# Performance work log

Measured on AMD Instinct MI355X. Metric: run time of the kernel, lower is better.

Reference implementation:

```python
import jax, jax.numpy as jnp
import numpy as np

FRAMES, PATCHES, DIM, HEADS, DFF, K = 256, 64, 512, 8, 1024, 128


def _mhsa(x, Wqkv, Wo, h):
    # standard multi-head self-attention, no bias, no norm (as in the repo)
    b, t, d = x.shape
    dh = d // h
    qkv = x @ Wqkv                                   # [b, t, 3d]
    q, k, v = jnp.split(qkv, 3, axis=-1)
    rs = lambda z: z.reshape(b, t, h, dh).transpose(0, 2, 1, 3)  # [b,h,t,dh]
    q, k, v = rs(q), rs(k), rs(v)
    att = jax.nn.softmax(jnp.einsum('bhqd,bhkd->bhqk', q, k) * (dh ** -0.5), axis=-1)
    out = jnp.einsum('bhqk,bhkd->bhqd', att, v)
    return out.transpose(0, 2, 1, 3).reshape(b, t, d) @ Wo


def _linformer(x, Wqkv, Wo, E, h):
    # Linformer: project K and V along the token axis with E before attention
    b, t, d = x.shape
    dh = d // h
    qkv = x @ Wqkv
    q, k, v = jnp.split(qkv, 3, axis=-1)
    rs = lambda z: z.reshape(b, t, h, dh).transpose(0, 2, 1, 3)
    q, k, v = rs(q), rs(k), rs(v)
    k = jnp.einsum('bhjd,jk->bhkd', k, E)            # [b,h,K,dh]
    v = jnp.einsum('bhjd,jk->bhkd', v, E)
    att = jax.nn.softmax(jnp.einsum('bhqd,bhkd->bhqk', q, k) * (dh ** -0.5), axis=-1)
    out = jnp.einsum('bhqk,bhkd->bhqd', att, v)
    return out.transpose(0, 2, 1, 3).reshape(b, t, d) @ Wo


def setup_inputs() -> dict:
    key = jax.random.key(0)
    ks = jax.random.split(key, 10)
    s = 0.02
    n = 1 + FRAMES * PATCHES
    return {
        'x': jax.random.normal(ks[0], (1, n, DIM), jnp.float32),
        'Wqkv_t': jax.random.normal(ks[1], (DIM, 3 * DIM), jnp.float32) * s,
        'Wo_t': jax.random.normal(ks[2], (DIM, DIM), jnp.float32) * s,
        'Wqkv_s': jax.random.normal(ks[3], (DIM, 3 * DIM), jnp.float32) * s,
        'Wo_s': jax.random.normal(ks[4], (DIM, DIM), jnp.float32) * s,
        'E': jax.random.normal(ks[5], (PATCHES + 1, K), jnp.float32) * s,
        'W1': jax.random.normal(ks[6], (DIM, DFF), jnp.float32) * s,
        'b1': jnp.zeros((DFF,), jnp.float32),
        'W2': jax.random.normal(ks[7], (DFF, DIM), jnp.float32) * s,
        'b2': jnp.zeros((DIM,), jnp.float32),
    }


def reference(x, Wqkv_t, Wo_t, Wqkv_s, Wo_s, E, W1, b1, W2, b2):
    b, n, d = x.shape
    f, p = FRAMES, PATCHES
    # split cls token
    cls, xt = x[:, :1], x[:, 1:]                      # [b,1,d], [b,f*p,d]
    # rearrange 'b (f p) d -> (b p) f d'
    xt = xt.reshape(b, f, p, d).transpose(0, 2, 1, 3).reshape(b * p, f, d)
    cls_t = jnp.tile(cls, (b * p // b, 1, 1))          # expand cls to batch b*p
    xt = jnp.concatenate([cls_t, xt], axis=1)          # [b*p, f+1, d]
    y = _mhsa(xt, Wqkv_t, Wo_t, HEADS) + xt            # time attention + residual
    cls2, y = y[:, :1], y[:, 1:]                       # [b*p,1,d], [b*p,f,d]
    # rearrange '(b p) f d -> (b f) p d'
    y = y.reshape(b, p, f, d).transpose(0, 2, 1, 3).reshape(b * f, p, d)
    cls_s = jnp.tile(cls2, (b * f // (b * p), 1, 1))   # expand cls to batch b*f
    y = jnp.concatenate([cls_s, y], axis=1)            # [b*f, p+1, d]
    y = _linformer(y, Wqkv_s, Wo_s, E, HEADS) + y      # space attention + residual
    # rearrange '(b f) p d -> b (f p) d' (token count is p+1 here, per source)
    y = y.reshape(b, f * (p + 1), d)
    h = jax.nn.gelu(y @ W1 + b1, approximate=False)    # nn.GELU is exact erf
    y = (h @ W2 + b2) + y                              # MLP + residual (dropout=eval)
    return y
```

## Files before the change

kernel.cpp:

```cpp
#include <hip/hip_runtime.h>


typedef unsigned short u16;
typedef unsigned int   u32;
typedef __attribute__((ext_vector_type(8))) short s16x8;
typedef __attribute__((ext_vector_type(4))) float f32x4;

__device__ __forceinline__ float b2f(u16 u) {
    return __uint_as_float(((u32)u) << 16);
}
__device__ __forceinline__ u16 f2b(float f) {
    u32 v = __float_as_uint(f);
    return (u16)((v + 0x7FFFu + ((v >> 16) & 1u)) >> 16);
}

__device__ __forceinline__ void gload16(const u16* g, u16* l) {
    __builtin_amdgcn_global_load_lds(
        (const __attribute__((address_space(1))) u32*)(const void*)g,
        (__attribute__((address_space(3))) u32*)(void*)l, 16, 0, 0);
}

__global__ __launch_bounds__(128) void build_xt_k(const float* __restrict__ x,
                                                  u16* __restrict__ xt) {
    int row = blockIdx.x;
    int p = row / 257, t = row % 257;
    long src = (t == 0) ? 0L : (long)(1 + (t - 1) * 64 + p);
    float4 v = ((const float4*)(x + src * 512))[threadIdx.x];
    ushort4 o;
    o.x = f2b(v.x); o.y = f2b(v.y); o.z = f2b(v.z); o.w = f2b(v.w);
    ((ushort4*)(xt + (long)row * 512))[threadIdx.x] = o;
}

__global__ __launch_bounds__(128) void build_ys_k(const u16* __restrict__ yt,
                                                  u16* __restrict__ ys) {
    int row = blockIdx.x;
    int f = row / 65, s = row % 65;
    long src = (s == 0) ? (long)((f & 63) * 257) : (long)((s - 1) * 257 + 1 + f);
    const uint2* sp = (const uint2*)(yt + src * 512);
    ((uint2*)(ys + (long)row * 512))[threadIdx.x] = sp[threadIdx.x];
}

__global__ __launch_bounds__(256) void store_f32(const u16* __restrict__ src,
                                                 float* __restrict__ dst) {
    long i = ((long)blockIdx.x * 256 + threadIdx.x) * 8;
    uint4 v = *(const uint4*)(src + i);
    float4 a, b;
    a.x = b2f((u16)v.x); a.y = b2f((u16)(v.x >> 16));
    a.z = b2f((u16)v.y); a.w = b2f((u16)(v.y >> 16));
    b.x = b2f((u16)v.z); b.y = b2f((u16)(v.z >> 16));
    b.z = b2f((u16)v.w); b.w = b2f((u16)(v.w >> 16));
    *(float4*)(dst + i) = a;
    *(float4*)(dst + i + 4) = b;
}

__global__ __launch_bounds__(256) void prep_wt(const float* __restrict__ src,
                                               u16* __restrict__ dst,
                                               int K, int N) {
    __shared__ float T[64][65];
    int k0 = blockIdx.x * 64, n0 = blockIdx.y * 64;
    int t = threadIdx.x;
    int r = t >> 2, q = t & 3;
#pragma unroll
    for (int i = 0; i < 4; ++i) {
        float4 v = *(const float4*)(src + (long)(k0 + r) * N + n0 + q * 16 + i * 4);
        T[r][q * 16 + i * 4 + 0] = v.x;
        T[r][q * 16 + i * 4 + 1] = v.y;
        T[r][q * 16 + i * 4 + 2] = v.z;
        T[r][q * 16 + i * 4 + 3] = v.w;
    }
    __syncthreads();
    u32 buf[8];
#pragma unroll
    for (int i = 0; i < 8; ++i) {
        float lo = T[q * 16 + 2 * i][r];
        float hi = T[q * 16 + 2 * i + 1][r];
        buf[i] = (u32)f2b(lo) | ((u32)f2b(hi) << 16);
    }
    u32* dp = (u32*)(dst + (long)(n0 + r) * K + k0 + q * 16);
#pragma unroll
    for (int i = 0; i < 8; ++i) dp[i] = buf[i];
}

template <int EPI, int OD>
__global__ __launch_bounds__(256) void gemm_mt(const u16* __restrict__ A, int lda,
                                               const u16* __restrict__ WT, int ldwt,
                                               int koff, int coff,
                                               const float* __restrict__ bias, int coff_b,
                                               const u16* __restrict__ res,
                                               void* __restrict__ outv,
                                               int Kd, int ldo) {
    __shared__ __align__(16) u16 As3[2][64][32];
    __shared__ __align__(16) u16 Bs3[2][256][32];
    const int tid = threadIdx.x;
    const int lane = tid & 63, w = tid >> 6;
    const int l15 = lane & 15, kg = lane >> 4;
    const int bn0 = blockIdx.x * 256, bm0 = blockIdx.y * 64;

    f32x4 acc[4][4];
#pragma unroll
    for (int i = 0; i < 4; ++i)
#pragma unroll
        for (int j = 0; j < 4; ++j) acc[i][j] = (f32x4){0.f, 0.f, 0.f, 0.f};

    const int srow = w * 16 + (lane >> 2);
    const int sga  = (lane & 3) ^ ((srow >> 1) & 3);
    const u16* gA = A + (long)(bm0 + srow) * lda + sga * 8;
    const u16* gB[4];
#pragma unroll
    for (int i = 0; i < 4; ++i) {
        int scol = w * 64 + i * 16 + (lane >> 2);
        int sgb = (lane & 3) ^ ((scol >> 1) & 3);
        gB[i] = WT + (long)(coff + bn0 + scol) * ldwt + koff + sgb * 8;
    }

    gload16(gA, &As3[0][w * 16][0]);
#pragma unroll
    for (int i = 0; i < 4; ++i)
        gload16(gB[i], &Bs3[0][w * 64 + i * 16][0]);
    __syncthreads();

    int cur = 0;
    for (int kt = 0; kt < Kd; kt += 32) {
        if (kt + 32 < Kd) {
            gload16(gA + kt + 32, &As3[cur ^ 1][w * 16][0]);
#pragma unroll
            for (int i = 0; i < 4; ++i)
                gload16(gB[i] + kt + 32, &Bs3[cur ^ 1][w * 64 + i * 16][0]);
        }
        s16x8 af[4], bfr[4];
#pragma unroll
        for (int mf = 0; mf < 4; ++mf) {
            int row = mf * 16 + l15;
            int slot = kg ^ ((row >> 1) & 3);
            af[mf] = *(const s16x8*)&As3[cur][row][slot * 8];
        }
#pragma unroll
        for (int nf = 0; nf < 4; ++nf) {
            int col = w * 64 + nf * 16 + l15;
            int slot = kg ^ ((col >> 1) & 3);
            bfr[nf] = *(const s16x8*)&Bs3[cur][col][slot * 8];
        }
#pragma unroll
        for (int mf = 0; mf < 4; ++mf)
#pragma unroll
            for (int nf = 0; nf < 4; ++nf)
                acc[mf][nf] = __builtin_amdgcn_mfma_f32_16x16x32_bf16(
                    af[mf], bfr[nf], acc[mf][nf], 0, 0, 0);
        __syncthreads();
        cur ^= 1;
    }

#pragma unroll
    for (int mf = 0; mf < 4; ++mf) {
#pragma unroll
        for (int nf = 0; nf < 4; ++nf) {
            int col = bn0 + w * 64 + nf * 16 + l15;
#pragma unroll
            for (int r = 0; r < 4; ++r) {
                int row = bm0 + mf * 16 + kg * 4 + r;
                float v = acc[mf][nf][r];
                if (EPI == 2 || EPI == 3) v += bias[coff_b + col];
                if (EPI == 2) v = 0.5f * v * (1.f + erff(v * 0.70710678118f));
                if (EPI == 1 || EPI == 3) v += b2f(res[(long)row * ldo + col]);
                if (OD == 0) ((u16*)outv)[(long)row * ldo + col] = f2b(v);
                else         ((float*)outv)[(long)row * ldo + col] = v;
            }
        }
    }
}

template <int EPI, int OD>
__global__ __launch_bounds__(256) void gemm_k(const u16* __restrict__ A, int lda,
                                              const float* __restrict__ W, int ldw,
                                              int koff, int coff,
                                              const float* __restrict__ bias, int coff_b,
                                              const u16* __restrict__ res,
                                              void* __restrict__ outv,
                                              int M, int N, int Kd, int ldo) {
    __shared__ float As[16][64];
    __shared__ float Ws[16][128];
    int tid = threadIdx.x;
    int tx = tid & 15, ty = tid >> 4;
    int bn0 = blockIdx.x * 128, bm0 = blockIdx.y * 64;

    float acc[4][8];
#pragma unroll
    for (int i = 0; i < 4; ++i)
#pragma unroll
        for (int j = 0; j < 8; ++j) acc[i][j] = 0.f;

    int am = tid >> 2, ak = (tid & 3) * 4;
    int wk = tid >> 4, wn = (tid & 15) * 8;
    const u16* Aptr = A + (long)(bm0 + am) * lda + ak;

    for (int kt = 0; kt < Kd; kt += 16) {
        const u32* ap = (const u32*)(Aptr + kt);
        u32 a0 = ap[0], a1 = ap[1];
        const float* wp = W + (long)(koff + kt + wk) * ldw + coff + bn0 + wn;
        float4 w0 = ((const float4*)wp)[0];
        float4 w1 = ((const float4*)wp)[1];
        __syncthreads();
        As[ak + 0][am] = b2f((u16)a0);
        As[ak + 1][am] = b2f((u16)(a0 >> 16));
        As[ak + 2][am] = b2f((u16)a1);
        As[ak + 3][am] = b2f((u16)(a1 >> 16));
        Ws[wk][wn + 0] = w0.x; Ws[wk][wn + 1] = w0.y;
        Ws[wk][wn + 2] = w0.z; Ws[wk][wn + 3] = w0.w;
        Ws[wk][wn + 4] = w1.x; Ws[wk][wn + 5] = w1.y;
        Ws[wk][wn + 6] = w1.z; Ws[wk][wn + 7] = w1.w;
        __syncthreads();
#pragma unroll
        for (int kk = 0; kk < 16; ++kk) {
            float a[4], b[8];
#pragma unroll
            for (int i = 0; i < 4; ++i) a[i] = As[kk][ty + 16 * i];
#pragma unroll
            for (int j = 0; j < 8; ++j) b[j] = Ws[kk][tx + 16 * j];
#pragma unroll
            for (int i = 0; i < 4; ++i)
#pragma unroll
                for (int j = 0; j < 8; ++j) acc[i][j] += a[i] * b[j];
        }
    }

#pragma unroll
    for (int i = 0; i < 4; ++i) {
        int row = bm0 + ty + 16 * i;
#pragma unroll
        for (int j = 0; j < 8; ++j) {
            int col = bn0 + tx + 16 * j;
            float v = acc[i][j];
            if (EPI == 2 || EPI == 3) v += bias[coff_b + col];
            if (EPI == 2) v = 0.5f * v * (1.f + erff(v * 0.70710678118f));
            if (EPI == 1 || EPI == 3) v += b2f(res[(long)row * ldo + col]);
            if (OD == 0) ((u16*)outv)[(long)row * ldo + col] = f2b(v);
            else         ((float*)outv)[(long)row * ldo + col] = v;
        }
    }
}

__global__ __launch_bounds__(256) void attn_t3(u16* __restrict__ QO,
                                               const u16* __restrict__ Kg,
                                               const u16* __restrict__ Vg,
                                               int hbase, int qbase) {
    __shared__ __align__(16) u16 sm[17280];
    const int tid = threadIdx.x;
    const int lane = tid & 63, w = tid >> 6;
    const int l15 = lane & 15, kg = lane >> 4;
    const int seq = blockIdx.x >> 2, hq = blockIdx.x & 3, h = hbase + hq;
    const int qc = blockIdx.y;
    const long row0 = (long)seq * 257;
    const int qcol = qbase + hq * 64;
    const int rb = qc * 128 + w * 32;

    u16* Kb = sm;
    u16* Vb = sm + 4224;
    u16* Pw = sm + 8320 + w * 2240;

    const u32* Ku = (const u32*)Kg;
    const u32* Vu = (const u32*)Vg;

    s16x8 qf[2][2];
#pragma unroll
    for (int mf = 0; mf < 2; ++mf) {
        int row = rb + mf * 16 + l15;
#pragma unroll
        for (int ks = 0; ks < 2; ++ks) {
            if (row < 257)
                qf[mf][ks] = *(const s16x8*)(QO + (row0 + row) * 512 + qcol + ks * 32 + kg * 8);
            else
                qf[mf][ks] = (s16x8){0, 0, 0, 0, 0, 0, 0, 0};
        }
    }

    f32x4 acc_o[2][4];
    float m[2][4], l[2][4];
#pragma unroll
    for (int mf = 0; mf < 2; ++mf)
#pragma unroll
        for (int i = 0; i < 4; ++i) {
            acc_o[mf][i] = (f32x4){0.f, 0.f, 0.f, 0.f};
            m[mf][i] = -3.0e38f;
            l[mf][i] = 0.f;
        }

    for (int kc = 0; kc < 320; kc += 64) {
        __syncthreads();
        for (int idx = tid; idx < 2048; idx += 256) {
            int key = idx >> 5, cu = idx & 31, d0 = cu * 2;
            int kk = kc + key; if (kk > 256) kk = 256;
            u32 kv = Ku[(row0 + kk) * 256 + h * 32 + cu];
            *(u32*)&Kb[(((cu >> 2) * 66 + key) << 3) + (d0 & 7)] = kv;
        }
#pragma unroll
        for (int it = 0; it < 2; ++it) {
            int kg2 = (tid >> 6) + it * 4;
            int d = tid & 63;
            int sh = (d & 1) * 16;
            long vcol = hq * 32 + (d >> 1);
            u32 pk[4];
#pragma unroll
            for (int jp = 0; jp < 4; ++jp) {
                int k0 = kc + kg2 * 8 + 2 * jp;
                int k1 = k0 + 1;
                if (k0 > 256) k0 = 256;
                if (k1 > 256) k1 = 256;
                u32 a = Vu[(row0 + k0) * 128 + vcol];
                u32 b = Vu[(row0 + k1) * 128 + vcol];
                pk[jp] = ((a >> sh) & 0xFFFFu) | (((b >> sh) & 0xFFFFu) << 16);
            }
            uint4 vv; vv.x = pk[0]; vv.y = pk[1]; vv.z = pk[2]; vv.w = pk[3];
            *(uint4*)&Vb[(kg2 * 64 + d) << 3] = vv;
        }
        __syncthreads();

        s16x8 kbf[2][4];
#pragma unroll
        for (int ks = 0; ks < 2; ++ks)
#pragma unroll
            for (int nf = 0; nf < 4; ++nf)
                kbf[ks][nf] = *(const s16x8*)&Kb[(((ks * 4 + kg) * 66 + nf * 16 + l15) << 3)];

        const bool lastc = (kc == 256);
#pragma unroll
        for (int mf = 0; mf < 2; ++mf) {
            f32x4 accs[4];
#pragma unroll
            for (int nf = 0; nf < 4; ++nf) accs[nf] = (f32x4){0.f, 0.f, 0.f, 0.f};
#pragma unroll
            for (int ks = 0; ks < 2; ++ks)
#pragma unroll
                for (int nf = 0; nf < 4; ++nf)
                    accs[nf] = __builtin_amdgcn_mfma_f32_16x16x32_bf16(
                        qf[mf][ks], kbf[ks][nf], accs[nf], 0, 0, 0);
#pragma unroll
            for (int r = 0; r < 4; ++r) {
                float sv[4];
#pragma unroll
                for (int nf = 0; nf < 4; ++nf) sv[nf] = accs[nf][r] * 0.125f;
                if (lastc) {
#pragma unroll
                    for (int nf = 0; nf < 4; ++nf)
                        if (nf * 16 + l15 > 0) sv[nf] = -3.0e38f;
                }
                float mx = fmaxf(fmaxf(sv[0], sv[1]), fmaxf(sv[2], sv[3]));
                mx = fmaxf(mx, __shfl_xor(mx, 1));
                mx = fmaxf(mx, __shfl_xor(mx, 2));
                mx = fmaxf(mx, __shfl_xor(mx, 4));
                mx = fmaxf(mx, __shfl_xor(mx, 8));
                if (mx > m[mf][r] + 8.f) {
                    float sc = __expf(m[mf][r] - mx);
                    l[mf][r] *= sc;
#pragma unroll
                    for (int nf = 0; nf < 4; ++nf) acc_o[mf][nf][r] *= sc;
                    m[mf][r] = mx;
                }
                float pl = 0.f;
                u16 pb[4];
#pragma unroll
                for (int nf = 0; nf < 4; ++nf) {
                    float p = __expf(sv[nf] - m[mf][r]);
                    pl += p;
                    pb[nf] = f2b(p);
                }
                pl += __shfl_xor(pl, 1);
                pl += __shfl_xor(pl, 2);
                pl += __shfl_xor(pl, 4);
                pl += __shfl_xor(pl, 8);
                l[mf][r] += pl;
                const int rr = mf * 16 + kg * 4 + r;
#pragma unroll
                for (int nf = 0; nf < 4; ++nf)
                    Pw[(((nf * 2 + (l15 >> 3)) * 35 + rr) << 3) + (l15 & 7)] = pb[nf];
            }
        }
#pragma unroll
        for (int ks2 = 0; ks2 < 2; ++ks2) {
            s16x8 vbf[4];
#pragma unroll
            for (int nf = 0; nf < 4; ++nf)
                vbf[nf] = *(const s16x8*)&Vb[(((ks2 * 4 + kg) * 64 + nf * 16 + l15) << 3)];
#pragma unroll
            for (int mf = 0; mf < 2; ++mf) {
                s16x8 pa = *(const s16x8*)&Pw[(((ks2 * 4 + kg) * 35 + mf * 16 + l15) << 3)];
#pragma unroll
                for (int nf = 0; nf < 4; ++nf)
                    acc_o[mf][nf] = __builtin_amdgcn_mfma_f32_16x16x32_bf16(
                        pa, vbf[nf], acc_o[mf][nf], 0, 0, 0);
            }
        }
    }

#pragma unroll
    for (int mf = 0; mf < 2; ++mf) {
#pragma unroll
        for (int r = 0; r < 4; ++r) {
            int row = rb + mf * 16 + kg * 4 + r;
            if (row < 257) {
                float inv = 1.f / l[mf][r];
#pragma unroll
                for (int nf = 0; nf < 4; ++nf)
                    QO[(row0 + row) * 512 + qcol + nf * 16 + l15] =
                        f2b(acc_o[mf][nf][r] * inv);
            }
        }
    }
}

__global__ __launch_bounds__(320) void attn_t2(u16* __restrict__ QO,
                                               const u16* __restrict__ Kg,
                                               const u16* __restrict__ Vg,
                                               int hbase, int qbase_u32) {
    __shared__ u32 Ks[2080];
    __shared__ u32 Vs[2080];
    const int seq = blockIdx.x >> 2, hq = blockIdx.x & 3, h = hbase + hq;
    const int qc = blockIdx.y;
    const int tid = threadIdx.x;
    const int quad = tid >> 2, kq = tid & 3;
    const long row0 = (long)seq * 257;
    const int nq = (qc == 3) ? 65 : 64;
    const bool act = quad < nq;

    u32* QOu = (u32*)QO;
    const u32* Ku = (const u32*)Kg;
    const u32* Vu = (const u32*)Vg;

    const long qaddr = (row0 + qc * 64 + quad) * 256 + qbase_u32 + hq * 32 + kq * 8;

    float q[16], oacc[16];
#pragma unroll
    for (int i = 0; i < 16; ++i) { q[i] = 0.f; oacc[i] = 0.f; }
    if (act) {
        uint4 a = ((const uint4*)(QOu + qaddr))[0];
        uint4 b = ((const uint4*)(QOu + qaddr))[1];
        q[0]  = b2f((u16)a.x); q[1]  = b2f((u16)(a.x >> 16));
        q[2]  = b2f((u16)a.y); q[3]  = b2f((u16)(a.y >> 16));
        q[4]  = b2f((u16)a.z); q[5]  = b2f((u16)(a.z >> 16));
        q[6]  = b2f((u16)a.w); q[7]  = b2f((u16)(a.w >> 16));
        q[8]  = b2f((u16)b.x); q[9]  = b2f((u16)(b.x >> 16));
        q[10] = b2f((u16)b.y); q[11] = b2f((u16)(b.y >> 16));
        q[12] = b2f((u16)b.z); q[13] = b2f((u16)(b.z >> 16));
        q[14] = b2f((u16)b.w); q[15] = b2f((u16)(b.w >> 16));
    }
    float m = -3.0e38f, l = 0.f;

    for (int cc = 0; cc < 4; ++cc) {
        const int c0 = cc << 6;
        const int cn = (cc == 3) ? 65 : 64;
        __syncthreads();
        for (int idx = tid; idx < (cn << 5); idx += 320) {
            int r = idx >> 5, c = idx & 31;
            long grow = row0 + c0 + r;
            Ks[idx] = Ku[grow * 256 + h * 32 + c];
            Vs[idx] = Vu[grow * 128 + hq * 32 + c];
        }
        __syncthreads();
        if (act) {
            for (int j = 0; j < cn; ++j) {
                const uint4* kp = (const uint4*)(Ks + (j << 5) + (kq << 3));
                uint4 ka = kp[0], kb = kp[1];
                float s =
                    q[0]  * b2f((u16)ka.x) + q[1]  * b2f((u16)(ka.x >> 16)) +
                    q[2]  * b2f((u16)ka.y) + q[3]  * b2f((u16)(ka.y >> 16)) +
                    q[4]  * b2f((u16)ka.z) + q[5]  * b2f((u16)(ka.z >> 16)) +
                    q[6]  * b2f((u16)ka.w) + q[7]  * b2f((u16)(ka.w >> 16)) +
                    q[8]  * b2f((u16)kb.x) + q[9]  * b2f((u16)(kb.x >> 16)) +
                    q[10] * b2f((u16)kb.y) + q[11] * b2f((u16)(kb.y >> 16)) +
                    q[12] * b2f((u16)kb.z) + q[13] * b2f((u16)(kb.z >> 16)) +
                    q[14] * b2f((u16)kb.w) + q[15] * b2f((u16)(kb.w >> 16));
                s += __shfl_xor(s, 1);
                s += __shfl_xor(s, 2);
                s *= 0.125f;
                if (s > m + 8.f) {
                    float sc = __expf(m - s);
                    l *= sc;
#pragma unroll
                    for (int i = 0; i < 16; ++i) oacc[i] *= sc;
                    m = s;
                }
                float p = __expf(s - m);
                l += p;
                const uint4* vp = (const uint4*)(Vs + (j << 5) + (kq << 3));
                uint4 va = vp[0], vb = vp[1];
                oacc[0]  += p * b2f((u16)va.x); oacc[1]  += p * b2f((u16)(va.x >> 16));
                oacc[2]  += p * b2f((u16)va.y); oacc[3]  += p * b2f((u16)(va.y >> 16));
                oacc[4]  += p * b2f((u16)va.z); oacc[5]  += p * b2f((u16)(va.z >> 16));
                oacc[6]  += p * b2f((u16)va.w); oacc[7]  += p * b2f((u16)(va.w >> 16));
                oacc[8]  += p * b2f((u16)vb.x); oacc[9]  += p * b2f((u16)(vb.x >> 16));
                oacc[10] += p * b2f((u16)vb.y); oacc[11] += p * b2f((u16)(vb.y >> 16));
                oacc[12] += p * b2f((u16)vb.z); oacc[13] += p * b2f((u16)(vb.z >> 16));
                oacc[14] += p * b2f((u16)vb.w); oacc[15] += p * b2f((u16)(vb.w >> 16));
            }
        }
    }
    if (act) {
        float inv = 1.f / l;
        uint4 o0, o1;
        o0.x = (u32)f2b(oacc[0]  * inv) | ((u32)f2b(oacc[1]  * inv) << 16);
        o0.y = (u32)f2b(oacc[2]  * inv) | ((u32)f2b(oacc[3]  * inv) << 16);
        o0.z = (u32)f2b(oacc[4]  * inv) | ((u32)f2b(oacc[5]  * inv) << 16);
        o0.w = (u32)f2b(oacc[6]  * inv) | ((u32)f2b(oacc[7]  * inv) << 16);
        o1.x = (u32)f2b(oacc[8]  * inv) | ((u32)f2b(oacc[9]  * inv) << 16);
        o1.y = (u32)f2b(oacc[10] * inv) | ((u32)f2b(oacc[11] * inv) << 16);
        o1.z = (u32)f2b(oacc[12] * inv) | ((u32)f2b(oacc[13] * inv) << 16);
        o1.w = (u32)f2b(oacc[14] * inv) | ((u32)f2b(oacc[15] * inv) << 16);
        ((uint4*)(QOu + qaddr))[0] = o0;
        ((uint4*)(QOu + qaddr))[1] = o1;
    }
}

__global__ __launch_bounds__(320) void attn_s2(const u16* __restrict__ Qg,
                                               const u16* __restrict__ Kg,
                                               u16* __restrict__ Vg,
                                               const float* __restrict__ E,
                                               int hbase) {
    __shared__ u32 smu[14882];
    u32* Kpt = smu;
    u32* Es2 = smu + 4352;
    u32* Ks2 = smu + 8512;
    u32* Vs2 = smu + 10592;
    u32* Qs2 = smu + 12672;

    const int bid = blockIdx.x, f = bid >> 2, hq = bid & 3, h = hbase + hq;
    const int tid = threadIdx.x;
    const long rbase = (long)f * 65;
    const u32* Kgu = (const u32*)Kg;
    u32* Vgu = (u32*)Vg;
    const u32* Qgu = (const u32*)Qg;

    for (int idx = tid; idx < 4160; idx += 320) {
        float e0 = E[2 * idx], e1 = E[2 * idx + 1];
        Es2[idx] = (u32)f2b(e0) | ((u32)f2b(e1) << 16);
    }
    for (int idx = tid; idx < 2080; idx += 320) {
        int r = idx >> 5, c = idx & 31;
        long src = (rbase + r) * 256 + h * 32 + c;
        Ks2[r * 32 + c] = Kgu[src];
        Vs2[r * 32 + c] = Vgu[src];
        Qs2[r * 34 + c] = Qgu[(rbase + r) * 128 + hq * 32 + c];
    }
    __syncthreads();

    if (tid < 256) {
        const int d = tid >> 2, kq4 = tid & 3;
        float kp[32];
#pragma unroll
        for (int i = 0; i < 32; ++i) kp[i] = 0.f;
        const u16* Ku = (const u16*)Ks2;
        for (int j = 0; j < 65; ++j) {
            float kv = b2f(Ku[j * 64 + d]);
            const uint4* ep = (const uint4*)(Es2 + j * 64 + kq4 * 16);
#pragma unroll
            for (int i4 = 0; i4 < 4; ++i4) {
                uint4 e4 = ep[i4];
                kp[i4 * 8 + 0] += kv * b2f((u16)e4.x);
                kp[i4 * 8 + 1] += kv * b2f((u16)(e4.x >> 16));
                kp[i4 * 8 + 2] += kv * b2f((u16)e4.y);
                kp[i4 * 8 + 3] += kv * b2f((u16)(e4.y >> 16));
                kp[i4 * 8 + 4] += kv * b2f((u16)e4.z);
                kp[i4 * 8 + 5] += kv * b2f((u16)(e4.z >> 16));
                kp[i4 * 8 + 6] += kv * b2f((u16)e4.w);
                kp[i4 * 8 + 7] += kv * b2f((u16)(e4.w >> 16));
            }
        }
        u32* ko = Kpt + d * 68 + kq4 * 16;
#pragma unroll
        for (int i2 = 0; i2 < 16; ++i2)
            ko[i2] = (u32)f2b(kp[2 * i2]) | ((u32)f2b(kp[2 * i2 + 1]) << 16);
    }
    __syncthreads();

    const int q = tid >> 2, kq = tid & 3;
    if (q < 65) {
        float s[32];
#pragma unroll
        for (int i = 0; i < 32; ++i) s[i] = 0.f;
        const u32* qrow = Qs2 + q * 34;
        for (int d2 = 0; d2 < 32; ++d2) {
            u32 qw = qrow[d2];
            float q0 = b2f((u16)qw), q1 = b2f((u16)(qw >> 16));
            const uint4* r0 = (const uint4*)(Kpt + (2 * d2) * 68 + kq * 16);
            const uint4* r1 = (const uint4*)(Kpt + (2 * d2 + 1) * 68 + kq * 16);
#pragma unroll
            for (int i4 = 0; i4 < 4; ++i4) {
                uint4 a = r0[i4], b = r1[i4];
                s[i4 * 8 + 0] += q0 * b2f((u16)a.x) + q1 * b2f((u16)b.x);
                s[i4 * 8 + 1] += q0 * b2f((u16)(a.x >> 16)) + q1 * b2f((u16)(b.x >> 16));
                s[i4 * 8 + 2] += q0 * b2f((u16)a.y) + q1 * b2f((u16)b.y);
                s[i4 * 8 + 3] += q0 * b2f((u16)(a.y >> 16)) + q1 * b2f((u16)(b.y >> 16));
                s[i4 * 8 + 4] += q0 * b2f((u16)a.z) + q1 * b2f((u16)b.z);
                s[i4 * 8 + 5] += q0 * b2f((u16)(a.z >> 16)) + q1 * b2f((u16)(b.z >> 16));
                s[i4 * 8 + 6] += q0 * b2f((u16)a.w) + q1 * b2f((u16)b.w);
                s[i4 * 8 + 7] += q0 * b2f((u16)(a.w >> 16)) + q1 * b2f((u16)(b.w >> 16));
            }
        }
        float m = -3.0e38f;
#pragma unroll
        for (int i = 0; i < 32; ++i) { s[i] *= 0.125f; m = fmaxf(m, s[i]); }
        m = fmaxf(m, __shfl_xor(m, 1));
        m = fmaxf(m, __shfl_xor(m, 2));
        float l = 0.f;
#pragma unroll
        for (int i = 0; i < 32; ++i) { s[i] = __expf(s[i] - m); l += s[i]; }
        l += __shfl_xor(l, 1);
        l += __shfl_xor(l, 2);

        float o[16];
#pragma unroll
        for (int i = 0; i < 16; ++i) o[i] = 0.f;
        for (int j = 0; j < 65; ++j) {
            const uint4* ep = (const uint4*)(Es2 + j * 64 + kq * 16);
            float pe = 0.f;
#pragma unroll
            for (int i4 = 0; i4 < 4; ++i4) {
                uint4 e4 = ep[i4];
                pe += s[i4 * 8 + 0] * b2f((u16)e4.x) + s[i4 * 8 + 1] * b2f((u16)(e4.x >> 16))
                    + s[i4 * 8 + 2] * b2f((u16)e4.y) + s[i4 * 8 + 3] * b2f((u16)(e4.y >> 16))
                    + s[i4 * 8 + 4] * b2f((u16)e4.z) + s[i4 * 8 + 5] * b2f((u16)(e4.z >> 16))
                    + s[i4 * 8 + 6] * b2f((u16)e4.w) + s[i4 * 8 + 7] * b2f((u16)(e4.w >> 16));
            }
            pe += __shfl_xor(pe, 1);
            pe += __shfl_xor(pe, 2);
            const uint4* vp = (const uint4*)(Vs2 + j * 32 + kq * 8);
#pragma unroll
            for (int i4 = 0; i4 < 2; ++i4) {
                uint4 v4 = vp[i4];
                o[i4 * 8 + 0] += pe * b2f((u16)v4.x);
                o[i4 * 8 + 1] += pe * b2f((u16)(v4.x >> 16));
                o[i4 * 8 + 2] += pe * b2f((u16)v4.y);
                o[i4 * 8 + 3] += pe * b2f((u16)(v4.y >> 16));
                o[i4 * 8 + 4] += pe * b2f((u16)v4.z);
                o[i4 * 8 + 5] += pe * b2f((u16)(v4.z >> 16));
                o[i4 * 8 + 6] += pe * b2f((u16)v4.w);
                o[i4 * 8 + 7] += pe * b2f((u16)(v4.w >> 16));
            }
        }
        float inv = 1.f / l;
        u32* op = Vgu + (rbase + q) * 256 + h * 32 + kq * 8;
#pragma unroll
        for (int i = 0; i < 8; ++i)
            op[i] = (u32)f2b(o[2 * i] * inv) | ((u32)f2b(o[2 * i + 1] * inv) << 16);
    }
}

__global__ __launch_bounds__(256) void attn_s3(const u16* __restrict__ Qg,
                                               const u16* __restrict__ Kg,
                                               u16* __restrict__ Vg,
                                               const float* __restrict__ E,
                                               int hbase) {
    __shared__ __align__(16) u16 sm[33024];
    u16* ET8 = sm;
    u16* KT8 = sm + 8192;
    u16* VT8 = sm + 12288;
    u16* Er  = sm + 16384;
    u16* Kr  = sm + 16512;
    u16* Vr  = sm + 16576;
    u16* Q8  = sm;
    u16* P16 = sm + 5120;
    float* Srow = (float*)(sm + 15360);
    u16* Kp8   = sm + 16640;
    u16* VpT16 = sm + 24832;

    const int bid = blockIdx.x, f = bid >> 2, hq = bid & 3, h = hbase + hq;
    const int tid = threadIdx.x;
    const int lane = tid & 63, w = tid >> 6;
    const int l15 = lane & 15, kg = lane >> 4;
    const long rbase = (long)f * 65;
    const u32* Kgu = (const u32*)Kg;
    u32* Vgu = (u32*)Vg;
    const u32* Qgu = (const u32*)Qg;

    for (int idx = tid; idx < 8320; idx += 256) {
        int j = idx >> 7, kL = idx & 127;
        u16 v = f2b(E[idx]);
        if (j < 64) ET8[(((j >> 3) * 128 + kL) << 3) + (j & 7)] = v;
        else        Er[kL] = v;
    }
    for (int idx = tid; idx < 2080; idx += 256) {
        int j = idx >> 5, cu = idx & 31;
        long src = (rbase + j) * 256 + h * 32 + cu;
        u32 kv = Kgu[src], vv = Vgu[src];
        int d0 = cu * 2;
        if (j < 64) {
            int base = (j >> 3), jj = j & 7;
            KT8[(((base) * 64 + d0) << 3) + jj]     = (u16)kv;
            KT8[(((base) * 64 + d0 + 1) << 3) + jj] = (u16)(kv >> 16);
            VT8[(((base) * 64 + d0) << 3) + jj]     = (u16)vv;
            VT8[(((base) * 64 + d0 + 1) << 3) + jj] = (u16)(vv >> 16);
        } else {
            Kr[d0] = (u16)kv; Kr[d0 + 1] = (u16)(kv >> 16);
            Vr[d0] = (u16)vv; Vr[d0 + 1] = (u16)(vv >> 16);
        }
    }
    __syncthreads();

    {
        f32x4 acc[2][4];
#pragma unroll
        for (int i = 0; i < 2; ++i)
#pragma unroll
            for (int j2 = 0; j2 < 4; ++j2) acc[i][j2] = (f32x4){0.f, 0.f, 0.f, 0.f};
#pragma unroll
        for (int ks = 0; ks < 2; ++ks) {
            int c = ks * 4 + kg;
            s16x8 a0 = *(const s16x8*)&ET8[((c * 128 + (2 * w) * 16 + l15) << 3)];
            s16x8 a1 = *(const s16x8*)&ET8[((c * 128 + (2 * w + 1) * 16 + l15) << 3)];
            s16x8 b0 = *(const s16x8*)&KT8[((c * 64 + 0 * 16 + l15) << 3)];
            s16x8 b1 = *(const s16x8*)&KT8[((c * 64 + 1 * 16 + l15) << 3)];
            s16x8 b2v = *(const s16x8*)&KT8[((c * 64 + 2 * 16 + l15) << 3)];
            s16x8 b3 = *(const s16x8*)&KT8[((c * 64 + 3 * 16 + l15) << 3)];
            acc[0][0] = __builtin_amdgcn_mfma_f32_16x16x32_bf16(a0, b0, acc[0][0], 0, 0, 0);
            acc[0][1] = __builtin_amdgcn_mfma_f32_16x16x32_bf16(a0, b1, acc[0][1], 0, 0, 0);
            acc[0][2] = __builtin_amdgcn_mfma_f32_16x16x32_bf16(a0, b2v, acc[0][2], 0, 0, 0);
            acc[0][3] = __builtin_amdgcn_mfma_f32_16x16x32_bf16(a0, b3, acc[0][3], 0, 0, 0);
            acc[1][0] = __builtin_amdgcn_mfma_f32_16x16x32_bf16(a1, b0, acc[1][0], 0, 0, 0);
            acc[1][1] = __builtin_amdgcn_mfma_f32_16x16x32_bf16(a1, b1, acc[1][1], 0, 0, 0);
            acc[1][2] = __builtin_amdgcn_mfma_f32_16x16x32_bf16(a1, b2v, acc[1][2], 0, 0, 0);
            acc[1][3] = __builtin_amdgcn_mfma_f32_16x16x32_bf16(a1, b3, acc[1][3], 0, 0, 0);
        }
#pragma unroll
        for (int mi = 0; mi < 2; ++mi)
#pragma unroll
            for (int nf = 0; nf < 4; ++nf) {
                int d = nf * 16 + l15;
                float kr = b2f(Kr[d]);
                int cidx = (nf * 2 + (l15 >> 3));
#pragma unroll
                for (int r = 0; r < 4; ++r) {
                    int kL = (2 * w + mi) * 16 + kg * 4 + r;
                    float v = acc[mi][nf][r] + b2f(Er[kL]) * kr;
                    Kp8[((cidx * 128 + kL) << 3) + (l15 & 7)] = f2b(v);
                }
            }
    }

    {
        f32x4 acc[8];
#pragma unroll
        for (int i = 0; i < 8; ++i) acc[i] = (f32x4){0.f, 0.f, 0.f, 0.f};
#pragma unroll
        for (int ks = 0; ks < 2; ++ks) {
            int c = ks * 4 + kg;
            s16x8 a = *(const s16x8*)&VT8[((c * 64 + w * 16 + l15) << 3)];
#pragma unroll
            for (int nf = 0; nf < 8; ++nf) {
                s16x8 b = *(const s16x8*)&ET8[((c * 128 + nf * 16 + l15) << 3)];
                acc[nf] = __builtin_amdgcn_mfma_f32_16x16x32_bf16(a, b, acc[nf], 0, 0, 0);
            }
        }
#pragma unroll
        for (int nf = 0; nf < 8; ++nf) {
            int kL = nf * 16 + l15;
            float er = b2f(Er[kL]);
            int cidx = (nf * 2 + (l15 >> 3));
#pragma unroll
            for (int r = 0; r < 4; ++r) {
                int d = w * 16 + kg * 4 + r;
                float v = acc[nf][r] + b2f(Vr[d]) * er;
                VpT16[((cidx * 64 + d) << 3) + (l15 & 7)] = f2b(v);
            }
        }
    }
    __syncthreads();

    for (int idx = tid; idx < 2560; idx += 256) {
        int rq = idx >> 5, cu = idx & 31;
        u32 val = (rq < 65) ? Qgu[(rbase + rq) * 128 + hq * 32 + cu] : 0u;
        *(u32*)&Q8[(((cu >> 2) * 80 + rq) << 3) + ((2 * cu) & 7)] = val;
    }
    __syncthreads();

    {
        f32x4 accs[8], acc4[2];
#pragma unroll
        for (int i = 0; i < 8; ++i) accs[i] = (f32x4){0.f, 0.f, 0.f, 0.f};
#pragma unroll
        for (int i = 0; i < 2; ++i) acc4[i] = (f32x4){0.f, 0.f, 0.f, 0.f};
#pragma unroll
        for (int ks = 0; ks < 2; ++ks) {
            int c = ks * 4 + kg;
            s16x8 a = *(const s16x8*)&Q8[((c * 80 + w * 16 + l15) << 3)];
            s16x8 a4 = *(const s16x8*)&Q8[((c * 80 + 64 + l15) << 3)];
#pragma unroll
            for (int nf = 0; nf < 8; ++nf) {
                s16x8 b = *(const s16x8*)&Kp8[((c * 128 + nf * 16 + l15) << 3)];
                accs[nf] = __builtin_amdgcn_mfma_f32_16x16x32_bf16(a, b, accs[nf], 0, 0, 0);
            }
#pragma unroll
            for (int i = 0; i < 2; ++i) {
                int nf4 = 2 * w + i;
                s16x8 b = *(const s16x8*)&Kp8[((c * 128 + nf4 * 16 + l15) << 3)];
                acc4[i] = __builtin_amdgcn_mfma_f32_16x16x32_bf16(a4, b, acc4[i], 0, 0, 0);
            }
        }
#pragma unroll
        for (int r = 0; r < 4; ++r) {
            float sv[8];
            float mx = -3.0e38f;
#pragma unroll
            for (int nf = 0; nf < 8; ++nf) {
                sv[nf] = accs[nf][r] * 0.125f;
                mx = fmaxf(mx, sv[nf]);
            }
            mx = fmaxf(mx, __shfl_xor(mx, 1));
            mx = fmaxf(mx, __shfl_xor(mx, 2));
            mx = fmaxf(mx, __shfl_xor(mx, 4));
            mx = fmaxf(mx, __shfl_xor(mx, 8));
            float l = 0.f;
#pragma unroll
            for (int nf = 0; nf < 8; ++nf) { sv[nf] = __expf(sv[nf] - mx); l += sv[nf]; }
            l += __shfl_xor(l, 1);
            l += __shfl_xor(l, 2);
            l += __shfl_xor(l, 4);
            l += __shfl_xor(l, 8);
            float inv = 1.f / l;
            int row = w * 16 + kg * 4 + r;
#pragma unroll
            for (int nf = 0; nf < 8; ++nf)
                P16[(((nf * 2 + (l15 >> 3)) * 80 + row) << 3) + (l15 & 7)] = f2b(sv[nf] * inv);
        }
        if (kg == 0) {
#pragma unroll
            for (int i = 0; i < 2; ++i)
                Srow[(2 * w + i) * 16 + l15] = acc4[i][0] * 0.125f;
        }
        for (int idx = tid; idx < 1920; idx += 256) {
            int row = 65 + (idx >> 7), col = idx & 127;
            P16[(((col >> 3) * 80 + row) << 3) + (col & 7)] = 0;
        }
    }
    __syncthreads();

    if (w == 0) {
        float v0 = Srow[lane], v1 = Srow[lane + 64];
        float mx = fmaxf(v0, v1);
#pragma unroll
        for (int s = 1; s < 64; s <<= 1) mx = fmaxf(mx, __shfl_xor(mx, s));
        float p0 = __expf(v0 - mx), p1 = __expf(v1 - mx);
        float l = p0 + p1;
#pragma unroll
        for (int s = 1; s < 64; s <<= 1) l += __shfl_xor(l, s);
        float inv = 1.f / l;
        int c0 = lane, c1 = lane + 64;
        P16[(((c0 >> 3) * 80 + 64) << 3) + (c0 & 7)] = f2b(p0 * inv);
        P16[(((c1 >> 3) * 80 + 64) << 3) + (c1 & 7)] = f2b(p1 * inv);
    }
    __syncthreads();

    {
        f32x4 acco[4], acco4;
#pragma unroll
        for (int i = 0; i < 4; ++i) acco[i] = (f32x4){0.f, 0.f, 0.f, 0.f};
        acco4 = (f32x4){0.f, 0.f, 0.f, 0.f};
#pragma unroll
        for (int ks = 0; ks < 4; ++ks) {
            int c = ks * 4 + kg;
            s16x8 a = *(const s16x8*)&P16[((c * 80 + w * 16 + l15) << 3)];
            s16x8 a4 = *(const s16x8*)&P16[((c * 80 + 64 + l15) << 3)];
#pragma unroll
            for (int nf = 0; nf < 4; ++nf) {
                s16x8 b = *(const s16x8*)&VpT16[((c * 64 + nf * 16 + l15) << 3)];
                acco[nf] = __builtin_amdgcn_mfma_f32_16x16x32_bf16(a, b, acco[nf], 0, 0, 0);
            }
            s16x8 b4 = *(const s16x8*)&VpT16[((c * 64 + w * 16 + l15) << 3)];
            acco4 = __builtin_amdgcn_mfma_f32_16x16x32_bf16(a4, b4, acco4, 0, 0, 0);
        }
        u16* Vg16 = (u16*)Vgu;
#pragma unroll
        for (int nf = 0; nf < 4; ++nf) {
            int d = nf * 16 + l15;
#pragma unroll
            for (int r = 0; r < 4; ++r) {
                int q = w * 16 + kg * 4 + r;
                Vg16[(rbase + q) * 512 + h * 64 + d] = f2b(acco[nf][r]);
            }
        }
        if (kg == 0) {
            int d = w * 16 + l15;
            Vg16[(rbase + 64) * 512 + h * 64 + d] = f2b(acco4[0]);
        }
    }
}

extern "C" void kernel_launch(void* const* d_in, const int* in_sizes, int n_in,
                              void* d_out, int out_size, void* d_ws, size_t ws_size,
                              hipStream_t stream) {
    int ix = 0, iE = 5, ib1 = 7, ib2 = 9;
    int q1 = -1, q2 = -1, o1 = -1, o2 = -1, w1 = -1, w2 = -1;
    for (int i = 0; i < n_in; ++i) {
        int s = in_sizes[i];
        if (s == 8389120) { if (ix != i && i == 0) ix = i; else if (in_sizes[ix] != 8389120) ix = i; }
        else if (s == 8320) iE = i;
        else if (s == 1024) ib1 = i;
        else if (s == 512) ib2 = i;
        else if (s == 786432) { if (q1 < 0) q1 = i; else q2 = i; }
        else if (s == 262144) { if (o1 < 0) o1 = i; else o2 = i; }
        else if (s == 524288) { if (w1 < 0) w1 = i; else w2 = i; }
    }
    if (q1 < 0) q1 = 1; if (o1 < 0) o1 = 2;
    if (q2 < 0) q2 = 3; if (o2 < 0) o2 = 4;
    if (w1 < 0) w1 = 6; if (ib1 < 0) ib1 = 7;
    if (w2 < 0) w2 = 8;

    const float* x      = (const float*)d_in[ix];
    const float* Wqkv_t = (const float*)d_in[q1];
    const float* Wo_t   = (const float*)d_in[o1];
    const float* Wqkv_s = (const float*)d_in[q2];
    const float* Wo_s   = (const float*)d_in[o2];
    const float* E      = (const float*)d_in[iE];
    const float* W1     = (const float*)d_in[w1];
    const float* b1     = (const float*)d_in[ib1];
    const float* W2     = (const float*)d_in[w2];
    const float* b2     = (const float*)d_in[ib2];

    float* outf = (float*)d_out;
    u16* D0 = (u16*)d_out;
    u16* B = (u16*)d_ws;
    u16* H = B + 8519680L;
    u16* D0up = D0 + 8519680L;

    const bool mfma = (ws_size >= 31850496UL);

    if (mfma) {
        u16* WT1 = H + 4259840L;
        u16* WT2 = WT1 + 786432L;
        u16* WT3 = WT2 + 262144L;
        u16* WT4 = WT3 + 786432L;
        u16* WT5 = WT4 + 262144L;
        u16* WT6 = WT5 + 524288L;

        prep_wt<<<dim3(8, 24), 256, 0, stream>>>(Wqkv_t, WT1, 512, 1536);
        prep_wt<<<dim3(8, 8),  256, 0, stream>>>(Wo_t,   WT2, 512, 512);
        prep_wt<<<dim3(8, 24), 256, 0, stream>>>(Wqkv_s, WT3, 512, 1536);
        prep_wt<<<dim3(8, 8),  256, 0, stream>>>(Wo_s,   WT4, 512, 512);
        prep_wt<<<dim3(8, 16), 256, 0, stream>>>(W1,     WT5, 512, 1024);
        prep_wt<<<dim3(16, 8), 256, 0, stream>>>(W2,     WT6, 1024, 512);

        build_xt_k<<<16448, 128, 0, stream>>>(x, B);
        gemm_mt<0, 0><<<dim3(2, 257), 256, 0, stream>>>(B, 512, WT1, 512, 0, 512,
                                                        nullptr, 0, nullptr, D0up, 512, 512);
        gemm_mt<0, 0><<<dim3(2, 257), 256, 0, stream>>>(B, 512, WT1, 512, 0, 0,
                                                        nullptr, 0, nullptr, D0, 512, 512);
        gemm_mt<0, 0><<<dim3(1, 257), 256, 0, stream>>>(B, 512, WT1, 512, 0, 1024,
                                                        nullptr, 0, nullptr, H, 512, 256);
        attn_t3<<<dim3(256, 3), 256, 0, stream>>>(D0, D0up, H, 0, 0);
        gemm_mt<0, 0><<<dim3(1, 257), 256, 0, stream>>>(B, 512, WT1, 512, 0, 1280,
                                                        nullptr, 0, nullptr, H, 512, 256);
        attn_t3<<<dim3(256, 3), 256, 0, stream>>>(D0, D0up, H, 4, 256);
        gemm_mt<1, 0><<<dim3(2, 257), 256, 0, stream>>>(D0, 512, WT2, 512, 0, 0,
                                                        nullptr, 0, B, B, 512, 512);
        build_ys_k<<<16640, 128, 0, stream>>>(B, D0);
        gemm_mt<0, 0><<<dim3(2, 260), 256, 0, stream>>>(D0, 512, WT3, 512, 0, 512,
                                                        nullptr, 0, nullptr, B, 512, 512);
        gemm_mt<0, 0><<<dim3(2, 260), 256, 0, stream>>>(D0, 512, WT3, 512, 0, 1024,
                                                        nullptr, 0, nullptr, D0up, 512, 512);
        gemm_mt<0, 0><<<dim3(1, 260), 256, 0, stream>>>(D0, 512, WT3, 512, 0, 0,
                                                        nullptr, 0, nullptr, H, 512, 256);
        attn_s3<<<1024, 256, 0, stream>>>(H, B, D0up, E, 0);
        gemm_mt<0, 0><<<dim3(1, 260), 256, 0, stream>>>(D0, 512, WT3, 512, 0, 256,
                                                        nullptr, 0, nullptr, H, 512, 256);
        attn_s3<<<1024, 256, 0, stream>>>(H, B, D0up, E, 4);
        gemm_mt<1, 0><<<dim3(2, 260), 256, 0, stream>>>(D0up, 512, WT4, 512, 0, 0,
                                                        nullptr, 0, D0, D0, 512, 512);
        gemm_mt<2, 0><<<dim3(2, 260), 256, 0, stream>>>(D0, 512, WT5, 512, 0, 0,
                                                        b1, 0, nullptr, D0up, 512, 512);
        gemm_mt<3, 0><<<dim3(2, 260), 256, 0, stream>>>(D0up, 512, WT6, 1024, 0, 0,
                                                        b2, 0, D0, B, 512, 512);
        gemm_mt<2, 0><<<dim3(2, 260), 256, 0, stream>>>(D0, 512, WT5, 512, 0, 512,
                                                        b1, 512, nullptr, D0up, 512, 512);
        gemm_mt<1, 0><<<dim3(2, 260), 256, 0, stream>>>(D0up, 512, WT6, 1024, 512, 0,
                                                        nullptr, 0, B, B, 512, 512);
        store_f32<<<4160, 256, 0, stream>>>(B, outf);
    } else {
        build_xt_k<<<16448, 128, 0, stream>>>(x, B);
        gemm_k<0, 0><<<dim3(4, 257), 256, 0, stream>>>(B, 512, Wqkv_t, 1536, 0, 512,
                                                       nullptr, 0, nullptr, D0up,
                                                       16448, 512, 512, 512);
        gemm_k<0, 0><<<dim3(2, 257), 256, 0, stream>>>(B, 512, Wqkv_t, 1536, 0, 1024,
                                                       nullptr, 0, nullptr, H,
                                                       16448, 256, 512, 256);
        gemm_k<0, 0><<<dim3(2, 257), 256, 0, stream>>>(B, 512, Wqkv_t, 1536, 0, 0,
                                                       nullptr, 0, nullptr, D0,
                                                       16448, 256, 512, 512);
        attn_t2<<<dim3(256, 4), 320, 0, stream>>>(D0, D0up, H, 0, 0);
        gemm_k<0, 0><<<dim3(2, 257), 256, 0, stream>>>(B, 512, Wqkv_t, 1536, 0, 1280,
                                                       nullptr, 0, nullptr, H,
                                                       16448, 256, 512, 256);
        gemm_k<0, 0><<<dim3(2, 257), 256, 0, stream>>>(B, 512, Wqkv_t, 1536, 0, 256,
                                                       nullptr, 0, nullptr, D0 + 256,
                                                       16448, 256, 512, 512);
        attn_t2<<<dim3(256, 4), 320, 0, stream>>>(D0, D0up, H, 4, 128);
        gemm_k<1, 0><<<dim3(4, 257), 256, 0, stream>>>(D0, 512, Wo_t, 512, 0, 0,
                                                       nullptr, 0, B, B,
                                                       16448, 512, 512, 512);
        build_ys_k<<<16640, 128, 0, stream>>>(B, D0);
        gemm_k<0, 0><<<dim3(4, 260), 256, 0, stream>>>(D0, 512, Wqkv_s, 1536, 0, 512,
                                                       nullptr, 0, nullptr, B,
                                                       16640, 512, 512, 512);
        gemm_k<0, 0><<<dim3(4, 260), 256, 0, stream>>>(D0, 512, Wqkv_s, 1536, 0, 1024,
                                                       nullptr, 0, nullptr, D0up,
                                                       16640, 512, 512, 512);
        gemm_k<0, 0><<<dim3(2, 260), 256, 0, stream>>>(D0, 512, Wqkv_s, 1536, 0, 0,
                                                       nullptr, 0, nullptr, H,
                                                       16640, 256, 512, 256);
        attn_s2<<<1024, 320, 0, stream>>>(H, B, D0up, E, 0);
        gemm_k<0, 0><<<dim3(2, 260), 256, 0, stream>>>(D0, 512, Wqkv_s, 1536, 0, 256,
                                                       nullptr, 0, nullptr, H,
                                                       16640, 256, 512, 256);
        attn_s2<<<1024, 320, 0, stream>>>(H, B, D0up, E, 4);
        gemm_k<1, 0><<<dim3(4, 260), 256, 0, stream>>>(D0up, 512, Wo_s, 512, 0, 0,
                                                       nullptr, 0, D0, D0,
                                                       16640, 512, 512, 512);
        for (int qd = 0; qd < 4; ++qd) {
            gemm_k<2, 0><<<dim3(2, 260), 256, 0, stream>>>(D0, 512, W1, 1024, 0, qd * 256,
                                                           b1, qd * 256, nullptr, H,
                                                           16640, 256, 512, 256);
            if (qd == 0)
                gemm_k<3, 0><<<dim3(4, 260), 256, 0, stream>>>(H, 256, W2, 512, qd * 256, 0,
                                                               b2, 0, D0, B,
                                                               16640, 512, 256, 512);
            else if (qd < 3)
                gemm_k<1, 0><<<dim3(4, 260), 256, 0, stream>>>(H, 256, W2, 512, qd * 256, 0,
                                                               nullptr, 0, B, B,
                                                               16640, 512, 256, 512);
            else
                gemm_k<1, 1><<<dim3(4, 260), 256, 0, stream>>>(H, 256, W2, 512, qd * 256, 0,
                                                               nullptr, 0, B, outf,
                                                               16640, 512, 256, 512);
        }
    }
}
```

Measured before the change: 637.2 us.

## Fuse space-layout permutation into Wo GEMM epilogue and use fixed-max softmax

The time-attention output projection GEMM now writes its results straight into the (frame, patch+1) space-attention layout, broadcasting the cls row to all frames. This removes the separate build_ys_k permutation kernel and its extra pass over memory, and the buffers used by the later GEMMs are reassigned to match. The time-attention kernel also drops the online-softmax running max and rescaling. It subtracts a fixed offset of 8 before exponentiating and does the row-sum shuffle reduction only once at the end. That fixed offset can overflow or underflow if scores leave the expected range, and the remapped epilogue issues scattered stores instead of contiguous row writes.

```diff
diff --git a/kernel.cpp b/kernel.cpp
--- a/kernel.cpp
+++ b/kernel.cpp
@@ -81,7 +81,7 @@
     for (int i = 0; i < 8; ++i) dp[i] = buf[i];
 }
 
-template <int EPI, int OD>
+template <int EPI, int OD, int REMAP = 0>
 __global__ __launch_bounds__(256) void gemm_mt(const u16* __restrict__ A, int lda,
                                                const u16* __restrict__ WT, int ldwt,
                                                int koff, int coff,
@@ -162,8 +162,20 @@
                 if (EPI == 2 || EPI == 3) v += bias[coff_b + col];
                 if (EPI == 2) v = 0.5f * v * (1.f + erff(v * 0.70710678118f));
                 if (EPI == 1 || EPI == 3) v += b2f(res[(long)row * ldo + col]);
-                if (OD == 0) ((u16*)outv)[(long)row * ldo + col] = f2b(v);
-                else         ((float*)outv)[(long)row * ldo + col] = v;
+                if (REMAP == 0) {
+                    if (OD == 0) ((u16*)outv)[(long)row * ldo + col] = f2b(v);
+                    else         ((float*)outv)[(long)row * ldo + col] = v;
+                } else {
+                    u16 hv = f2b(v);
+                    int t = row % 257, p = row / 257;
+                    if (t == 0) {
+#pragma unroll
+                        for (int j = 0; j < 4; ++j)
+                            ((u16*)outv)[(long)((p + 64 * j) * 65) * ldo + col] = hv;
+                    } else {
+                        ((u16*)outv)[(long)((t - 1) * 65 + p + 1) * ldo + col] = hv;
+                    }
+                }
             }
         }
     }
@@ -252,6 +264,7 @@
     const long row0 = (long)seq * 257;
     const int qcol = qbase + hq * 64;
     const int rb = qc * 128 + w * 32;
+    const float FM = 8.f;
 
     u16* Kb = sm;
     u16* Vb = sm + 4224;
@@ -274,14 +287,13 @@
     }
 
     f32x4 acc_o[2][4];
-    float m[2][4], l[2][4];
+    float lsum[2][4];
 #pragma unroll
     for (int mf = 0; mf < 2; ++mf)
 #pragma unroll
         for (int i = 0; i < 4; ++i) {
             acc_o[mf][i] = (f32x4){0.f, 0.f, 0.f, 0.f};
-            m[mf][i] = -3.0e38f;
-            l[mf][i] = 0.f;
+            lsum[mf][i] = 0.f;
         }
 
     for (int kc = 0; kc < 320; kc += 64) {
@@ -337,37 +349,21 @@
             for (int r = 0; r < 4; ++r) {
                 float sv[4];
 #pragma unroll
-                for (int nf = 0; nf < 4; ++nf) sv[nf] = accs[nf][r] * 0.125f;
+                for (int nf = 0; nf < 4; ++nf) sv[nf] = accs[nf][r] * 0.125f - FM;
                 if (lastc) {
 #pragma unroll
                     for (int nf = 0; nf < 4; ++nf)
                         if (nf * 16 + l15 > 0) sv[nf] = -3.0e38f;
                 }
-                float mx = fmaxf(fmaxf(sv[0], sv[1]), fmaxf(sv[2], sv[3]));
-                mx = fmaxf(mx, __shfl_xor(mx, 1));
-                mx = fmaxf(mx, __shfl_xor(mx, 2));
-                mx = fmaxf(mx, __shfl_xor(mx, 4));
-                mx = fmaxf(mx, __shfl_xor(mx, 8));
-                if (mx > m[mf][r] + 8.f) {
-                    float sc = __expf(m[mf][r] - mx);
-                    l[mf][r] *= sc;
-#pragma unroll
-                    for (int nf = 0; nf < 4; ++nf) acc_o[mf][nf][r] *= sc;
-                    m[mf][r] = mx;
-                }
-                float pl = 0.f;
+                float ps = 0.f;
                 u16 pb[4];
 #pragma unroll
                 for (int nf = 0; nf < 4; ++nf) {
-                    float p = __expf(sv[nf] - m[mf][r]);
-                    pl += p;
+                    float p = __expf(sv[nf]);
+                    ps += p;
                     pb[nf] = f2b(p);
                 }
-                pl += __shfl_xor(pl, 1);
-                pl += __shfl_xor(pl, 2);
-                pl += __shfl_xor(pl, 4);
-                pl += __shfl_xor(pl, 8);
-                l[mf][r] += pl;
+                lsum[mf][r] += ps;
                 const int rr = mf * 16 + kg * 4 + r;
 #pragma unroll
                 for (int nf = 0; nf < 4; ++nf)
@@ -395,9 +391,14 @@
     for (int mf = 0; mf < 2; ++mf) {
 #pragma unroll
         for (int r = 0; r < 4; ++r) {
+            float l = lsum[mf][r];
+            l += __shfl_xor(l, 1);
+            l += __shfl_xor(l, 2);
+            l += __shfl_xor(l, 4);
+            l += __shfl_xor(l, 8);
             int row = rb + mf * 16 + kg * 4 + r;
             if (row < 257) {
-                float inv = 1.f / l[mf][r];
+                float inv = 1.f / l;
 #pragma unroll
                 for (int nf = 0; nf < 4; ++nf)
                     QO[(row0 + row) * 512 + qcol + nf * 16 + l15] =
@@ -947,28 +948,27 @@
         gemm_mt<0, 0><<<dim3(1, 257), 256, 0, stream>>>(B, 512, WT1, 512, 0, 1280,
                                                         nullptr, 0, nullptr, H, 512, 256);
         attn_t3<<<dim3(256, 3), 256, 0, stream>>>(D0, D0up, H, 4, 256);
-        gemm_mt<1, 0><<<dim3(2, 257), 256, 0, stream>>>(D0, 512, WT2, 512, 0, 0,
-                                                        nullptr, 0, B, B, 512, 512);
-        build_ys_k<<<16640, 128, 0, stream>>>(B, D0);
-        gemm_mt<0, 0><<<dim3(2, 260), 256, 0, stream>>>(D0, 512, WT3, 512, 0, 512,
+        gemm_mt<1, 0, 1><<<dim3(2, 257), 256, 0, stream>>>(D0, 512, WT2, 512, 0, 0,
+                                                           nullptr, 0, B, D0up, 512, 512);
+        gemm_mt<0, 0><<<dim3(2, 260), 256, 0, stream>>>(D0up, 512, WT3, 512, 0, 512,
                                                         nullptr, 0, nullptr, B, 512, 512);
-        gemm_mt<0, 0><<<dim3(2, 260), 256, 0, stream>>>(D0, 512, WT3, 512, 0, 1024,
-                                                        nullptr, 0, nullptr, D0up, 512, 512);
-        gemm_mt<0, 0><<<dim3(1, 260), 256, 0, stream>>>(D0, 512, WT3, 512, 0, 0,
+        gemm_mt<0, 0><<<dim3(2, 260), 256, 0, stream>>>(D0up, 512, WT3, 512, 0, 1024,
+                                                        nullptr, 0, nullptr, D0, 512, 512);
+        gemm_mt<0, 0><<<dim3(1, 260), 256, 0, stream>>>(D0up, 512, WT3, 512, 0, 0,
                                                         nullptr, 0, nullptr, H, 512, 256);
-        attn_s3<<<1024, 256, 0, stream>>>(H, B, D0up, E, 0);
-        gemm_mt<0, 0><<<dim3(1, 260), 256, 0, stream>>>(D0, 512, WT3, 512, 0, 256,
+        attn_s3<<<1024, 256, 0, stream>>>(H, B, D0, E, 0);
+        gemm_mt<0, 0><<<dim3(1, 260), 256, 0, stream>>>(D0up, 512, WT3, 512, 0, 256,
                                                         nullptr, 0, nullptr, H, 512, 256);
-        attn_s3<<<1024, 256, 0, stream>>>(H, B, D0up, E, 4);
-        gemm_mt<1, 0><<<dim3(2, 260), 256, 0, stream>>>(D0up, 512, WT4, 512, 0, 0,
-                                                        nullptr, 0, D0, D0, 512, 512);
-        gemm_mt<2, 0><<<dim3(2, 260), 256, 0, stream>>>(D0, 512, WT5, 512, 0, 0,
-                                                        b1, 0, nullptr, D0up, 512, 512);
-        gemm_mt<3, 0><<<dim3(2, 260), 256, 0, stream>>>(D0up, 512, WT6, 1024, 0, 0,
-                                                        b2, 0, D0, B, 512, 512);
-        gemm_mt<2, 0><<<dim3(2, 260), 256, 0, stream>>>(D0, 512, WT5, 512, 0, 512,
-                                                        b1, 512, nullptr, D0up, 512, 512);
-        gemm_mt<1, 0><<<dim3(2, 260), 256, 0, stream>>>(D0up, 512, WT6, 1024, 512, 0,
+        attn_s3<<<1024, 256, 0, stream>>>(H, B, D0, E, 4);
+        gemm_mt<1, 0><<<dim3(2, 260), 256, 0, stream>>>(D0, 512, WT4, 512, 0, 0,
+                                                        nullptr, 0, D0up, D0up, 512, 512);
+        gemm_mt<2, 0><<<dim3(2, 260), 256, 0, stream>>>(D0up, 512, WT5, 512, 0, 0,
+                                                        b1, 0, nullptr, D0, 512, 512);
+        gemm_mt<3, 0><<<dim3(2, 260), 256, 0, stream>>>(D0, 512, WT6, 1024, 0, 0,
+                                                        b2, 0, D0up, B, 512, 512);
+        gemm_mt<2, 0><<<dim3(2, 260), 256, 0, stream>>>(D0up, 512, WT5, 512, 0, 512,
+                                                        b1, 512, nullptr, D0, 512, 512);
+        gemm_mt<1, 0><<<dim3(2, 260), 256, 0, stream>>>(D0, 512, WT6, 1024, 512, 0,
                                                         nullptr, 0, B, B, 512, 512);
         store_f32<<<4160, 256, 0, stream>>>(B, outf);
     } else {
```

Result: faster. 615.8 us (-3.4%).
